# Optimization experiments

Hardware: AMD Instinct MI355X
Metric: run time of the kernel (lower is better)

## Reference

```python
import jax, jax.numpy as jnp
import numpy as np

HEADS = 8
DIM_HEAD = 64
H = W = 32  # height = width = int(sqrt(num_patches)) = 32; n = 1024 tokens
N = H * W
TABLE = (2 * H - 1) * (2 * W - 1)  # 3969
NEG_THRESH = 0.9
GATE = -2.0  # non-trainable gate parameter


def _build_rel_index_dis():
    # valid 2D relative-position index in [0, TABLE) and normalized squared distance
    coords = np.stack(np.meshgrid(np.arange(H), np.arange(W), indexing='ij'))  # (2,H,W)
    flat = coords.reshape(2, -1)  # (2, N)
    rel = flat[:, :, None] - flat[:, None, :]  # (2, N, N)
    dis = (rel[0] / H) ** 2 + (rel[1] / W) ** 2
    idx = (rel[0] + H - 1) * (2 * W - 1) + (rel[1] + W - 1)
    return idx.astype(np.int32), dis.astype(np.float32)


def setup_inputs() -> dict:
    key = jax.random.key(0)
    ks = jax.random.split(key, 8)
    b, n, dim = 4, N, 512
    inner = HEADS * DIM_HEAD
    rel_index, dis = _build_rel_index_dis()
    return {
        'x': jax.random.normal(ks[0], (b, n, dim), jnp.float32),
        'prob': jax.random.uniform(ks[1], (b, n), jnp.float32),
        'W_qkv': jax.random.normal(ks[2], (dim, 3 * inner), jnp.float32) * 0.02,
        'table1': jax.random.normal(ks[3], (TABLE, HEADS), jnp.float32) * 0.02,
        'table2': jax.random.normal(ks[4], (TABLE, HEADS), jnp.float32) * 0.02,
        'headsita': jnp.arange(1, HEADS + 1, dtype=jnp.float32) * 0.1,
        'W_thresh': jax.random.normal(ks[5], (DIM_HEAD, 1), jnp.float32) * 0.02,
        'W_out': jax.random.normal(ks[6], (inner, 512), jnp.float32) * 0.02,
        'b_out': jnp.zeros((512,), jnp.float32),
        'rel_index': jnp.asarray(rel_index),
        'dis': jnp.asarray(dis),
    }


def reference(x, prob, W_qkv, table1, table2, headsita, W_thresh, W_out, b_out, rel_index, dis):
    b, n, dim = x.shape
    scale = DIM_HEAD ** -0.5
    qkv = x @ W_qkv  # (b, n, 3*inner)
    q, k, v = jnp.split(qkv, 3, axis=-1)
    split_heads = lambda t: t.reshape(b, n, HEADS, DIM_HEAD).transpose(0, 2, 1, 3)
    q, k, v = split_heads(q), split_heads(k), split_heads(v)  # (b, h, n, d)

    dots0 = jnp.einsum('bhid,bhjd->bhij', q, k) * scale  # (b, h, n, n)

    # dual RPE bias: product of two table gathers with shared index -> (h, n, n)
    bias = (table1[rel_index] * table2[rel_index]).transpose(2, 0, 1)
    factor = 1.0 / (2.0 * headsita ** 2 + 1e-6)  # (h,)
    pos_embed = jnp.exp(-factor[:, None, None] * dis[None, :, :])  # (h, n, n)
    dots = dots0 + bias[None] + 0.01 * pos_embed[None]

    attn = jax.nn.softmax(dots, axis=-1)
    attn_max = jnp.max(attn, axis=-1)  # (b, h, n)
    attn_min = jnp.min(attn, axis=-1)

    # per-query dynamic threshold, gated
    thresh_raw = jax.nn.sigmoid(jnp.einsum('bhnd,do->bhn', q, W_thresh)) * jax.nn.sigmoid(GATE)
    thresh = attn_min + thresh_raw * (attn_max - attn_min)  # (b, h, n)

    record = (attn - thresh[..., None] > 0).astype(attn.dtype)  # (b, h, n, n)
    # zero out query rows where prob >= NEG_THRESH
    record = jnp.where(prob[:, None, :, None] >= NEG_THRESH, 0.0, record)

    deno = jnp.einsum('bhij,bhij->bhi', attn, record)
    attn_pruned = attn * record / (deno[..., None] + 1e-6)

    out = jnp.einsum('bhij,bhjd->bhid', attn_pruned, v)  # (b, h, n, d)
    out = out.transpose(0, 2, 1, 3).reshape(b, n, HEADS * DIM_HEAD)
    out = out @ W_out + b_out
    attn0 = jax.nn.softmax(dots0, axis=-1)
    return out, attn0
```

## Files before the change

kernel.cpp:

```cpp
#include <hip/hip_runtime.h>
#include <cmath>

#define NTOK 1024
#define NH 8
#define DH 64
#define BATCH 4
#define TBL 3969

#define L2E 1.4426950408889634f

typedef __attribute__((ext_vector_type(8))) short short8;
typedef __attribute__((ext_vector_type(4))) float f32x4;

__device__ __forceinline__ unsigned bf16rne(float x) {
  unsigned u = __float_as_uint(x);
  return (u + 0x7fffu + ((u >> 16) & 1u)) >> 16;
}

__device__ __forceinline__ void cvt2(float a, float b, unsigned& h, unsigned& l) {
  asm("v_cvt_pk_bf16_f32 %0, %1, %2" : "=v"(h) : "v"(a), "v"(b));
  float ra = a - __uint_as_float(h << 16);
  float rb = b - __uint_as_float(h & 0xffff0000u);
  asm("v_cvt_pk_bf16_f32 %0, %1, %2" : "=v"(l) : "v"(ra), "v"(rb));
}

__device__ __forceinline__ void split8_pk(const float* v, short8& h8, short8& l8) {
  union { short8 s; unsigned u[4]; } H, L;
#pragma unroll
  for (int j = 0; j < 4; ++j) {
    unsigned hp, lp;
    cvt2(v[2 * j], v[2 * j + 1], hp, lp);
    H.u[j] = hp; L.u[j] = lp;
  }
  h8 = H.s; l8 = L.s;
}

__device__ __forceinline__ f32x4 mfma16(short8 a, short8 b, f32x4 c) {
  return __builtin_amdgcn_mfma_f32_16x16x32_bf16(a, b, c, 0, 0, 0);
}

__device__ __forceinline__ void gload16(const unsigned short* g, unsigned short* l) {
  __builtin_amdgcn_global_load_lds(
      (__attribute__((address_space(1))) unsigned int*)(g),
      (__attribute__((address_space(3))) unsigned int*)(l), 16, 0, 0);
}

__global__ void k_comb(const float* __restrict__ t1, const float* __restrict__ t2,
                       const float* __restrict__ sita, const float* __restrict__ dis,
                       float* __restrict__ comb, float* __restrict__ combe) {
  int idx = blockIdx.x * 256 + threadIdx.x;
  if (idx >= TBL) return;
  int dy = idx / 63 - 31, dx = idx % 63 - 31;
  int yi = dy > 0 ? dy : 0, yj = dy > 0 ? 0 : -dy;
  int xi = dx > 0 ? dx : 0, xj = dx > 0 ? 0 : -dx;
  float dv = dis[(size_t)(yi * 32 + xi) * NTOK + (yj * 32 + xj)];
#pragma unroll
  for (int h = 0; h < NH; ++h) {
    float ita = sita[h];
    float factor = 1.0f / (2.0f * ita * ita + 1e-6f);
    float bi = t1[idx * 8 + h] * t2[idx * 8 + h];
    float v = bi + 0.01f * expf(-factor * dv);
    comb[(size_t)h * TBL + idx] = v * L2E;
    combe[(size_t)h * TBL + idx] = expf(v);
  }
}

__global__ __launch_bounds__(256) void k_prep(
    const float* __restrict__ x, const float* __restrict__ wqkv,
    const float* __restrict__ wout,
    unsigned short* __restrict__ xh, unsigned short* __restrict__ xl,
    unsigned short* __restrict__ wth, unsigned short* __restrict__ wtl,
    unsigned short* __restrict__ wouth, unsigned short* __restrict__ woutl) {
  const int bid = blockIdx.x;
  const int t = threadIdx.x;
  if (bid < 1024) {
    size_t base = ((size_t)bid * 256 + t) * 8;
    float v8[8];
    *(float4*)(v8) = *(const float4*)(x + base);
    *(float4*)(v8 + 4) = *(const float4*)(x + base + 4);
    short8 h8, l8;
    split8_pk(v8, h8, l8);
    *(short8*)(xh + base) = h8;
    *(short8*)(xl + base) = l8;
    return;
  }
  __shared__ float tile[64][65];
  const float* src;
  unsigned short *dh, *dl;
  int n0, k0, N;
  if (bid < 1216) {
    int b2 = bid - 1024;
    n0 = (b2 % 24) * 64; k0 = (b2 / 24) * 64; N = 1536;
    src = wqkv; dh = wth; dl = wtl;
  } else {
    int b2 = bid - 1216;
    n0 = (b2 % 8) * 64; k0 = (b2 / 8) * 64; N = 512;
    src = wout; dh = wouth; dl = woutl;
  }
#pragma unroll
  for (int l = 0; l < 4; ++l) {
    int idx = t + l * 256;
    int r = idx >> 4, c4 = idx & 15;
    float4 v = *(const float4*)(src + (size_t)(k0 + r) * N + n0 + c4 * 4);
    tile[r][c4 * 4 + 0] = v.x; tile[r][c4 * 4 + 1] = v.y;
    tile[r][c4 * 4 + 2] = v.z; tile[r][c4 * 4 + 3] = v.w;
  }
  __syncthreads();
#pragma unroll
  for (int l = 0; l < 2; ++l) {
    int idx = t + l * 256;
    int n = idx >> 3, c8 = idx & 7;
    float v8[8];
#pragma unroll
    for (int j = 0; j < 8; ++j) v8[j] = tile[c8 * 8 + j][n];
    short8 h8, l8;
    split8_pk(v8, h8, l8);
    *(short8*)(dh + (size_t)(n0 + n) * 512 + k0 + c8 * 8) = h8;
    *(short8*)(dl + (size_t)(n0 + n) * 512 + k0 + c8 * 8) = l8;
  }
}

__device__ __forceinline__ void gemm_core(
    const unsigned short* pAh, const unsigned short* pAl,
    const unsigned short* pBh, const unsigned short* pBl,
    int a0, int b0, int w, int lane, f32x4 acc[4][4],
    unsigned short* AhS, unsigned short* AlS,
    unsigned short* BhS, unsigned short* BlS) {
  const int q = lane >> 4, li = lane & 15;
  const int wr = w >> 1, wc = w & 1;
#pragma unroll 1
  for (int k0 = 0; k0 < 512; k0 += 64) {
#pragma unroll
    for (int l = 0; l < 4; ++l) {
      int idx = w * 256 + l * 64 + lane;
      int row = idx >> 3, u = idx & 7;
      int so = k0 + ((u ^ (row & 7)) * 8);
      int db = (w * 256 + l * 64) * 8;
      gload16(pAh + (size_t)(a0 + row) * 512 + so, AhS + db);
      gload16(pAl + (size_t)(a0 + row) * 512 + so, AlS + db);
      gload16(pBh + (size_t)(b0 + row) * 512 + so, BhS + db);
      gload16(pBl + (size_t)(b0 + row) * 512 + so, BlS + db);
    }
    __syncthreads();
#pragma unroll
    for (int c = 0; c < 2; ++c) {
      short8 aH[4], aL[4], bH[4], bL[4];
#pragma unroll
      for (int mt = 0; mt < 4; ++mt) {
        int row = 64 * wr + 16 * mt + li;
        int ro = row * 64 + (((4 * c + q) ^ (row & 7)) * 8);
        aH[mt] = *(const short8*)(AhS + ro);
        aL[mt] = *(const short8*)(AlS + ro);
        int rowb = 64 * wc + 16 * mt + li;
        int rob = rowb * 64 + (((4 * c + q) ^ (rowb & 7)) * 8);
        bH[mt] = *(const short8*)(BhS + rob);
        bL[mt] = *(const short8*)(BlS + rob);
      }
#pragma unroll
      for (int mt = 0; mt < 4; ++mt)
#pragma unroll
        for (int nt = 0; nt < 4; ++nt) {
          acc[mt][nt] = mfma16(aH[mt], bH[nt], acc[mt][nt]);
          acc[mt][nt] = mfma16(aH[mt], bL[nt], acc[mt][nt]);
          acc[mt][nt] = mfma16(aL[mt], bH[nt], acc[mt][nt]);
        }
    }
    __syncthreads();
  }
}

__global__ __launch_bounds__(256, 2) void k_qkv(
    const unsigned short* __restrict__ xh, const unsigned short* __restrict__ xl,
    const unsigned short* __restrict__ wth, const unsigned short* __restrict__ wtl,
    float* __restrict__ qf, unsigned short* __restrict__ kspl,
    unsigned short* __restrict__ vspl) {
  __shared__ unsigned short AhS[8192], AlS[8192], BhS[8192], BlS[8192];
  const int bid = blockIdx.x;
  const int lin = (bid & 7) * 48 + (bid >> 3);
  const int by = lin / 12, bx = lin % 12;
  const int part = bx >> 2;
  const int t = threadIdx.x;
  const int w = t >> 6, lane = t & 63;
  const int q = lane >> 4, li = lane & 15;
  const int wr = w >> 1, wc = w & 1;
  f32x4 acc[4][4] = {};
  if (part < 2)
    gemm_core(wth, wtl, xh, xl, bx * 128, by * 128, w, lane, acc, AhS, AlS, BhS, BlS);
  else
    gemm_core(xh, xl, wth, wtl, by * 128, bx * 128, w, lane, acc, AhS, AlS, BhS, BlS);

  if (part == 0) {
    int hq = bx * 2 + wr;
#pragma unroll
    for (int nt = 0; nt < 4; ++nt) {
      int tok = by * 128 + 64 * wc + 16 * nt + li;
      int b = tok >> 10, i = tok & 1023;
#pragma unroll
      for (int mt = 0; mt < 4; ++mt) {
        int d0 = 16 * mt + 4 * q;
        float4 v;
        v.x = acc[mt][nt][0]; v.y = acc[mt][nt][1];
        v.z = acc[mt][nt][2]; v.w = acc[mt][nt][3];
        *(float4*)(qf + ((size_t)(b * NH + hq) * NTOK + i) * DH + d0) = v;
      }
    }
  } else if (part == 1) {
    int hq = bx * 2 + wr - 8;
#pragma unroll
    for (int nt = 0; nt < 4; ++nt) {
      int tok = by * 128 + 64 * wc + 16 * nt + li;
      int b = tok >> 10, tile = (tok & 1023) >> 6, tl = tok & 63;
      unsigned short* kb = kspl + ((size_t)((b * NH + hq) * 16 + tile) * 2) * 4096;
#pragma unroll
      for (int mt = 0; mt < 4; ++mt) {
        int d0 = 16 * mt + 4 * q;
        int pu = (d0 >> 3) ^ (tl & 7), off = d0 & 7;
        unsigned h0, h1, l0, l1;
        cvt2(acc[mt][nt][0], acc[mt][nt][1], h0, l0);
        cvt2(acc[mt][nt][2], acc[mt][nt][3], h1, l1);
        *(uint2*)(kb + tl * 64 + pu * 8 + off) = make_uint2(h0, h1);
        *(uint2*)(kb + 4096 + tl * 64 + pu * 8 + off) = make_uint2(l0, l1);
      }
    }
  } else {
    int hq = (bx - 8) * 2 + wc;
#pragma unroll
    for (int mt = 0; mt < 4; ++mt) {
      int tok0 = by * 128 + 64 * wr + 16 * mt + 4 * q;
      int b = tok0 >> 10, tile = (tok0 & 1023) >> 6, tl0 = tok0 & 63;
      int lu = tl0 >> 3, off = tl0 & 7;
#pragma unroll
      for (int nt = 0; nt < 4; ++nt) {
        int d = 16 * nt + li;
        unsigned short* vb = vspl + ((size_t)((b * NH + hq) * 16 + tile) * 2) * 4096;
        int pu = lu ^ (d & 7);
        unsigned h0, h1, l0, l1;
        cvt2(acc[mt][nt][0], acc[mt][nt][1], h0, l0);
        cvt2(acc[mt][nt][2], acc[mt][nt][3], h1, l1);
        *(uint2*)(vb + d * 64 + pu * 8 + off) = make_uint2(h0, h1);
        *(uint2*)(vb + 4096 + d * 64 + pu * 8 + off) = make_uint2(l0, l1);
      }
    }
  }
}

__global__ __launch_bounds__(512, 4) void k_attn(
    const float* __restrict__ qf, const unsigned short* __restrict__ kspl,
    const unsigned short* __restrict__ vspl, const float* __restrict__ prob,
    const float* __restrict__ comb, const float* __restrict__ combe,
    const float* __restrict__ wt,
    float* __restrict__ attn0, unsigned short* __restrict__ oh,
    unsigned short* __restrict__ ol) {
  __shared__ unsigned short KhS[4096], KlS[4096];
  __shared__ unsigned short VhS[4096], VlS[4096];
  __shared__ float PfS[64 * 68];
  __shared__ float2 csS[3 * 64];
  __shared__ float thrS[64];

  const int bid = blockIdx.x;
  const int lin = (bid & 7) * 64 + (bid >> 3);
  const int bh = lin >> 4;
  const int rt = lin & 15;
  const int b = bh >> 3, h = bh & 7;
  const int i0 = rt * 64;
  const int t = threadIdx.x;
  const int w = t >> 6;
  const int lane = t & 63;
  const int q = lane >> 4, li = lane & 15;
  const int g = w >> 1;
  const int cw = w & 1;
  const float* qb = qf + (size_t)bh * NTOK * DH;
  const float* ch = comb + (size_t)h * TBL;
  const float* che = combe + (size_t)h * TBL;
  const int rbase = (i0 >> 5) + 30;

  {
    int row = t >> 3, dg = t & 7;
    const float* qr2 = qb + (size_t)(i0 + row) * DH + dg * 8;
    float sum = 0.f;
#pragma unroll
    for (int c = 0; c < 8; ++c) sum += qr2[c] * wt[dg * 8 + c];
    sum += __shfl_xor(sum, 1);
    sum += __shfl_xor(sum, 2);
    sum += __shfl_xor(sum, 4);
    if (dg == 0)
      thrS[row] = (1.0f / (1.0f + exp2f(-sum * L2E))) * 0.11920292202211755f;
  }

  short8 qah[2], qal[2];
  {
    const float* qr2 = qb + (size_t)(i0 + 16 * g + li) * DH;
    const float QS = 0.125f * L2E;
#pragma unroll
    for (int c = 0; c < 2; ++c) {
      float4 a = *(const float4*)(qr2 + 32 * c + 8 * q);
      float4 bb = *(const float4*)(qr2 + 32 * c + 8 * q + 4);
      float tmp[8] = {a.x * QS, a.y * QS, a.z * QS, a.w * QS,
                      bb.x * QS, bb.y * QS, bb.z * QS, bb.w * QS};
      split8_pk(tmp, qah[c], qal[c]);
    }
  }

  float m0l[4], s0l[4], ml[4], sl[4], mnl[4];
#pragma unroll
  for (int r = 0; r < 4; ++r) {
    m0l[r] = -1e30f; ml[r] = -1e30f; mnl[r] = 1e30f;
    s0l[r] = 0.f; sl[r] = 0.f;
  }

#pragma unroll 1
  for (int j0 = 0; j0 < NTOK; j0 += 64) {
    const unsigned short* gk = kspl + ((size_t)(bh * 16 + (j0 >> 6)) * 2) * 4096;
    gload16(gk + w * 512 + lane * 8, KhS + w * 512);
    gload16(gk + 4096 + w * 512 + lane * 8, KlS + w * 512);
    if (t < 192) {
      int rl2 = t >> 6, c2 = t & 63;
      if (c2 < 63) {
        int off = (rbase - (j0 >> 5) + rl2) * 63 + c2;
        csS[rl2 * 64 + c2] = make_float2(ch[off], che[off]);
      }
    }
    __syncthreads();

    f32x4 acc2[2] = {};
#pragma unroll
    for (int c = 0; c < 2; ++c) {
#pragma unroll
      for (int T2 = 0; T2 < 2; ++T2) {
        int T = 2 * cw + T2;
        int ro = (16 * T + li) * 64 + ((4 * c + q) ^ (li & 7)) * 8;
        short8 bh8 = *(const short8*)(KhS + ro);
        short8 bl8 = *(const short8*)(KlS + ro);
        acc2[T2] = mfma16(qah[c], bh8, acc2[T2]);
        acc2[T2] = mfma16(qah[c], bl8, acc2[T2]);
        acc2[T2] = mfma16(qal[c], bh8, acc2[T2]);
      }
    }

    float2 ce[2][4];
    float t0[4], tt[4], tmn[4];
#pragma unroll
    for (int r = 0; r < 4; ++r) { t0[r] = -1e30f; tt[r] = -1e30f; tmn[r] = 1e30f; }
#pragma unroll
    for (int T2 = 0; T2 < 2; ++T2) {
      int jj = 16 * (2 * cw + T2) + li;
#pragma unroll
      for (int r = 0; r < 4; ++r) {
        int il = 16 * g + 4 * q + r;
        int rl2 = (il >> 5) - (jj >> 5) + 1;
        int cc2 = (il & 31) - (jj & 31) + 31;
        ce[T2][r] = csS[rl2 * 64 + cc2];
        float d0 = acc2[T2][r];
        float dt = d0 + ce[T2][r].x;
        t0[r] = fmaxf(t0[r], d0);
        tt[r] = fmaxf(tt[r], dt);
        tmn[r] = fminf(tmn[r], dt);
      }
    }
#pragma unroll
    for (int r = 0; r < 4; ++r) {
      float nm0 = fmaxf(m0l[r], t0[r]);
      float nm = fmaxf(ml[r], tt[r]);
      float sc0 = exp2f(m0l[r] - nm0), sc = exp2f(ml[r] - nm), k0 = exp2f(nm0 - nm);
      float s0a = 0.f, sEa = 0.f;
#pragma unroll
      for (int T2 = 0; T2 < 2; ++T2) {
        float e0 = exp2f(acc2[T2][r] - nm0);
        s0a += e0;
        sEa += e0 * ce[T2][r].y;
      }
      s0l[r] = s0l[r] * sc0 + s0a;
      sl[r] = sl[r] * sc + sEa * k0;
      m0l[r] = nm0; ml[r] = nm; mnl[r] = fminf(mnl[r], tmn[r]);
    }
    __syncthreads();
  }

  float M0[4], S0[4], M[4], S[4], MN[4];
#pragma unroll
  for (int r = 0; r < 4; ++r) {
    float m0v = m0l[r], s0 = s0l[r], m = ml[r], s = sl[r], mn = mnl[r];
#pragma unroll
    for (int off = 1; off < 16; off <<= 1) {
      float om = __shfl_xor(m0v, off), os = __shfl_xor(s0, off);
      float n0 = fmaxf(m0v, om);
      s0 = s0 * exp2f(m0v - n0) + os * exp2f(om - n0);
      m0v = n0;
      float om2 = __shfl_xor(m, off), os2 = __shfl_xor(s, off);
      float n2 = fmaxf(m, om2);
      s = s * exp2f(m - n2) + os2 * exp2f(om2 - n2);
      m = n2;
      mn = fminf(mn, __shfl_xor(mn, off));
    }
    M0[r] = m0v; S0[r] = s0; M[r] = m; S[r] = s; MN[r] = mn;
  }
  if (li == 0) {
#pragma unroll
    for (int r = 0; r < 4; ++r) {
      int row = 16 * g + 4 * q + r;
      float* p = PfS + (cw * 64 + row) * 5;
      p[0] = M0[r]; p[1] = S0[r]; p[2] = M[r]; p[3] = S[r]; p[4] = MN[r];
    }
  }
  __syncthreads();

  float m0f[4], is0f[4], thf[4], crf[4];
#pragma unroll
  for (int r = 0; r < 4; ++r) {
    int rloc = 16 * g + 4 * q + r;
    const float* pa = PfS + rloc * 5;
    const float* pb = PfS + (64 + rloc) * 5;
    float m0v = fmaxf(pa[0], pb[0]);
    float s0 = pa[1] * exp2f(pa[0] - m0v) + pb[1] * exp2f(pb[0] - m0v);
    float m = fmaxf(pa[2], pb[2]);
    float s = pa[3] * exp2f(pa[2] - m) + pb[3] * exp2f(pb[2] - m);
    float mn = fminf(pa[4], pb[4]);
    float isf = 1.f / s;
    float amin = exp2f(mn - m) * isf;
    float th = amin + thrS[rloc] * (isf - amin);
    if (prob[b * NTOK + i0 + rloc] >= 0.9f) th = 1e30f;
    m0f[r] = m0v; is0f[r] = 1.f / s0; thf[r] = th; crf[r] = exp2f(m0v - m) * isf;
  }
  __syncthreads();

  f32x4 oacc[4] = {};
  float denl[4] = {0.f, 0.f, 0.f, 0.f};
#pragma unroll 1
  for (int j0 = 0; j0 < NTOK; j0 += 64) {
    const unsigned short* gk = kspl + ((size_t)(bh * 16 + (j0 >> 6)) * 2) * 4096;
    const unsigned short* gv = vspl + ((size_t)(bh * 16 + (j0 >> 6)) * 2) * 4096;
    gload16(gk + w * 512 + lane * 8, KhS + w * 512);
    gload16(gk + 4096 + w * 512 + lane * 8, KlS + w * 512);
    gload16(gv + w * 512 + lane * 8, VhS + w * 512);
    gload16(gv + 4096 + w * 512 + lane * 8, VlS + w * 512);
    if (t < 192) {
      int rl2 = t >> 6, c2 = t & 63;
      if (c2 < 63) {
        int off = (rbase - (j0 >> 5) + rl2) * 63 + c2;
        csS[rl2 * 64 + c2] = make_float2(ch[off], che[off]);
      }
    }
    __syncthreads();

    f32x4 acc2[2] = {};
#pragma unroll
    for (int c = 0; c < 2; ++c) {
#pragma unroll
      for (int T2 = 0; T2 < 2; ++T2) {
        int T = 2 * cw + T2;
        int ro = (16 * T + li) * 64 + ((4 * c + q) ^ (li & 7)) * 8;
        short8 bh8 = *(const short8*)(KhS + ro);
        short8 bl8 = *(const short8*)(KlS + ro);
        acc2[T2] = mfma16(qah[c], bh8, acc2[T2]);
        acc2[T2] = mfma16(qah[c], bl8, acc2[T2]);
        acc2[T2] = mfma16(qal[c], bh8, acc2[T2]);
      }
    }

#pragma unroll
    for (int T2 = 0; T2 < 2; ++T2) {
      int jj = 16 * (2 * cw + T2) + li;
#pragma unroll
      for (int r = 0; r < 4; ++r) {
        int il = 16 * g + 4 * q + r;
        int rl2 = (il >> 5) - (jj >> 5) + 1;
        int cc2 = (il & 31) - (jj & 31) + 31;
        float ey = csS[rl2 * 64 + cc2].y;
        float e0 = exp2f(acc2[T2][r] - m0f[r]);
        __builtin_nontemporal_store(
            e0 * is0f[r],
            attn0 + (size_t)(bh * NTOK + i0 + il) * NTOK + j0 + jj);
        float at = e0 * ey * crf[r];
        float p = (at - thf[r] > 0.f) ? at : 0.f;
        denl[r] += p;
        PfS[il * 68 + jj] = p;
      }
    }
    {
      const float* pp = PfS + (16 * g + li) * 68 + 32 * cw + 8 * q;
      float pv8[8];
      *(float4*)(pv8) = *(const float4*)pp;
      *(float4*)(pv8 + 4) = *(const float4*)(pp + 4);
      short8 pah, pal;
      split8_pk(pv8, pah, pal);
#pragma unroll
      for (int T = 0; T < 4; ++T) {
        int ro = (16 * T + li) * 64 + ((4 * cw + q) ^ (li & 7)) * 8;
        short8 vh8 = *(const short8*)(VhS + ro);
        short8 vl8 = *(const short8*)(VlS + ro);
        oacc[T] = mfma16(pah, vh8, oacc[T]);
        oacc[T] = mfma16(pah, vl8, oacc[T]);
        oacc[T] = mfma16(pal, vh8, oacc[T]);
      }
    }
    __syncthreads();
  }

#pragma unroll
  for (int r = 0; r < 4; ++r) {
#pragma unroll
    for (int off = 1; off < 16; off <<= 1) denl[r] += __shfl_xor(denl[r], off);
  }
  if (cw == 1) {
#pragma unroll
    for (int r = 0; r < 4; ++r) {
      int row = 16 * g + 4 * q + r;
#pragma unroll
      for (int T = 0; T < 4; ++T) PfS[row * 68 + 16 * T + li] = oacc[T][r];
      if (li == 0) PfS[row * 68 + 64] = denl[r];
    }
  }
  __syncthreads();
  if (cw == 0) {
#pragma unroll
    for (int r = 0; r < 4; ++r) {
      int rloc = 16 * g + 4 * q + r;
      float dsum = denl[r] + PfS[rloc * 68 + 64];
      float pf = 1.f / (dsum + 1e-6f);
      int row = i0 + rloc;
      size_t rb2 = ((size_t)b * NTOK + row) * 512 + h * 64;
#pragma unroll
      for (int T = 0; T < 4; ++T) {
        float val = (oacc[T][r] + PfS[rloc * 68 + 16 * T + li]) * pf;
        unsigned hv = bf16rne(val);
        float lo2 = val - __uint_as_float(hv << 16);
        oh[rb2 + 16 * T + li] = (unsigned short)hv;
        ol[rb2 + 16 * T + li] = (unsigned short)bf16rne(lo2);
      }
    }
  }
}

__global__ __launch_bounds__(256, 2) void k_out(
    const unsigned short* __restrict__ wouth, const unsigned short* __restrict__ woutl,
    const unsigned short* __restrict__ oh, const unsigned short* __restrict__ ol,
    const float* __restrict__ bias, float* __restrict__ c) {
  __shared__ unsigned short AhS[8192], AlS[8192], BhS[8192], BlS[8192];
  const int bid = blockIdx.x;
  const int lin = (bid & 7) * 16 + (bid >> 3);
  const int by = lin >> 2, bx = lin & 3;
  const int t = threadIdx.x;
  const int w = t >> 6, lane = t & 63;
  const int q = lane >> 4, li = lane & 15;
  const int wr = w >> 1, wc = w & 1;
  f32x4 acc[4][4] = {};
  gemm_core(wouth, woutl, oh, ol, bx * 128, by * 128, w, lane, acc, AhS, AlS, BhS, BlS);
#pragma unroll
  for (int mt = 0; mt < 4; ++mt) {
    int col0 = bx * 128 + 64 * wr + 16 * mt + 4 * q;
    float4 b4 = *(const float4*)(bias + col0);
#pragma unroll
    for (int nt = 0; nt < 4; ++nt) {
      int tok = by * 128 + 64 * wc + 16 * nt + li;
      float4 v;
      v.x = acc[mt][nt][0] + b4.x; v.y = acc[mt][nt][1] + b4.y;
      v.z = acc[mt][nt][2] + b4.z; v.w = acc[mt][nt][3] + b4.w;
      *(float4*)(c + (size_t)tok * 512 + col0) = v;
    }
  }
}

extern "C" void kernel_launch(void* const* d_in, const int* in_sizes, int n_in,
                              void* d_out, int out_size, void* d_ws, size_t ws_size,
                              hipStream_t stream) {
  const float* x    = (const float*)d_in[0];
  const float* prob = (const float*)d_in[1];
  const float* wqkv = (const float*)d_in[2];
  const float* t1   = (const float*)d_in[3];
  const float* t2   = (const float*)d_in[4];
  const float* sita = (const float*)d_in[5];
  const float* wt   = (const float*)d_in[6];
  const float* wout = (const float*)d_in[7];
  const float* bout = (const float*)d_in[8];
  const float* dis  = (const float*)d_in[10];

  float* out = (float*)d_out;
  float* attn0 = out + (size_t)BATCH * NTOK * 512;

  float* comb = (float*)d_ws;
  float* combe = comb + 32768;
  float* qf = combe + 32768;
  unsigned short* kspl = (unsigned short*)(qf + (size_t)BATCH * NH * NTOK * DH);
  unsigned short* vspl = kspl + (size_t)4194304;
  unsigned short* xh = vspl + (size_t)4194304;
  unsigned short* xl = xh + (size_t)2097152;
  unsigned short* wth = xl + (size_t)2097152;
  unsigned short* wtl = wth + (size_t)786432;
  unsigned short* wouth = wtl + (size_t)786432;
  unsigned short* woutl = wouth + (size_t)262144;
  unsigned short* oh = xh;
  unsigned short* ol = xl;

  hipLaunchKernelGGL(k_comb, dim3(16), dim3(256), 0, stream, t1, t2, sita, dis, comb, combe);
  hipLaunchKernelGGL(k_prep, dim3(1280), dim3(256), 0, stream,
                     x, wqkv, wout, xh, xl, wth, wtl, wouth, woutl);
  hipLaunchKernelGGL(k_qkv, dim3(384), dim3(256), 0, stream,
                     xh, xl, wth, wtl, qf, kspl, vspl);
  hipLaunchKernelGGL(k_attn, dim3(512), dim3(512), 0, stream,
                     qf, kspl, vspl, prob, comb, combe, wt, attn0, oh, ol);
  hipLaunchKernelGGL(k_out, dim3(128), dim3(256), 0, stream,
                     wouth, woutl, oh, ol, bout, out);
}
```

Measured before the change: 280.5 us.

## Fuse comb into prep, shrink GEMM tiles, stage attn0 stores through LDS

Folds the comb table kernel into the prep kernel as extra blocks, which removes one launch. Templates the split-bf16 GEMM core so the QKV and output GEMMs can use 64x128 tiles, doubling grid sizes and raising the occupancy hint to 3 so the device has more blocks in flight. The attention kernel now writes the attn0 softmax tile into LDS and then issues coalesced 32-byte nontemporal row stores, instead of scattered per-element stores. It also hoists the relative-position table address math out of the inner loop. The costs are extra LDS use in k_attn, an added barrier, and less data reuse per GEMM tile.

```diff
diff --git a/kernel.cpp b/kernel.cpp
--- a/kernel.cpp
+++ b/kernel.cpp
@@ -45,34 +45,35 @@
       (__attribute__((address_space(3))) unsigned int*)(l), 16, 0, 0);
 }
 
-__global__ void k_comb(const float* __restrict__ t1, const float* __restrict__ t2,
-                       const float* __restrict__ sita, const float* __restrict__ dis,
-                       float* __restrict__ comb, float* __restrict__ combe) {
-  int idx = blockIdx.x * 256 + threadIdx.x;
-  if (idx >= TBL) return;
-  int dy = idx / 63 - 31, dx = idx % 63 - 31;
-  int yi = dy > 0 ? dy : 0, yj = dy > 0 ? 0 : -dy;
-  int xi = dx > 0 ? dx : 0, xj = dx > 0 ? 0 : -dx;
-  float dv = dis[(size_t)(yi * 32 + xi) * NTOK + (yj * 32 + xj)];
-#pragma unroll
-  for (int h = 0; h < NH; ++h) {
-    float ita = sita[h];
-    float factor = 1.0f / (2.0f * ita * ita + 1e-6f);
-    float bi = t1[idx * 8 + h] * t2[idx * 8 + h];
-    float v = bi + 0.01f * expf(-factor * dv);
-    comb[(size_t)h * TBL + idx] = v * L2E;
-    combe[(size_t)h * TBL + idx] = expf(v);
-  }
-}
-
 __global__ __launch_bounds__(256) void k_prep(
     const float* __restrict__ x, const float* __restrict__ wqkv,
     const float* __restrict__ wout,
     unsigned short* __restrict__ xh, unsigned short* __restrict__ xl,
     unsigned short* __restrict__ wth, unsigned short* __restrict__ wtl,
-    unsigned short* __restrict__ wouth, unsigned short* __restrict__ woutl) {
+    unsigned short* __restrict__ wouth, unsigned short* __restrict__ woutl,
+    const float* __restrict__ t1, const float* __restrict__ t2,
+    const float* __restrict__ sita, const float* __restrict__ dis,
+    float* __restrict__ comb, float* __restrict__ combe) {
   const int bid = blockIdx.x;
   const int t = threadIdx.x;
+  if (bid >= 1280) {
+    int idx = (bid - 1280) * 256 + t;
+    if (idx >= TBL) return;
+    int dy = idx / 63 - 31, dx = idx % 63 - 31;
+    int yi = dy > 0 ? dy : 0, yj = dy > 0 ? 0 : -dy;
+    int xi = dx > 0 ? dx : 0, xj = dx > 0 ? 0 : -dx;
+    float dv = dis[(size_t)(yi * 32 + xi) * NTOK + (yj * 32 + xj)];
+#pragma unroll
+    for (int h = 0; h < NH; ++h) {
+      float ita = sita[h];
+      float factor = 1.0f / (2.0f * ita * ita + 1e-6f);
+      float bi = t1[idx * 8 + h] * t2[idx * 8 + h];
+      float v = bi + 0.01f * expf(-factor * dv);
+      comb[(size_t)h * TBL + idx] = v * L2E;
+      combe[(size_t)h * TBL + idx] = expf(v);
+    }
+    return;
+  }
   if (bid < 1024) {
     size_t base = ((size_t)bid * 256 + t) * 8;
     float v8[8];
@@ -120,46 +121,58 @@
   }
 }
 
+template <int AR, int BR>
 __device__ __forceinline__ void gemm_core(
-    const unsigned short* pAh, const unsigned short* pAl,
-    const unsigned short* pBh, const unsigned short* pBl,
-    int a0, int b0, int w, int lane, f32x4 acc[4][4],
+    const unsigned short* __restrict__ pAh, const unsigned short* __restrict__ pAl,
+    const unsigned short* __restrict__ pBh, const unsigned short* __restrict__ pBl,
+    int a0, int b0, int t, f32x4 acc[AR / 32][BR / 32],
     unsigned short* AhS, unsigned short* AlS,
     unsigned short* BhS, unsigned short* BlS) {
+  constexpr int MT = AR / 32, NT = BR / 32;
+  const int lane = t & 63;
+  const int w = t >> 6;
   const int q = lane >> 4, li = lane & 15;
   const int wr = w >> 1, wc = w & 1;
 #pragma unroll 1
   for (int k0 = 0; k0 < 512; k0 += 64) {
 #pragma unroll
-    for (int l = 0; l < 4; ++l) {
-      int idx = w * 256 + l * 64 + lane;
+    for (int l = 0; l < AR / 32; ++l) {
+      int idx = l * 256 + t;
       int row = idx >> 3, u = idx & 7;
       int so = k0 + ((u ^ (row & 7)) * 8);
-      int db = (w * 256 + l * 64) * 8;
-      gload16(pAh + (size_t)(a0 + row) * 512 + so, AhS + db);
-      gload16(pAl + (size_t)(a0 + row) * 512 + so, AlS + db);
-      gload16(pBh + (size_t)(b0 + row) * 512 + so, BhS + db);
-      gload16(pBl + (size_t)(b0 + row) * 512 + so, BlS + db);
+      gload16(pAh + (size_t)(a0 + row) * 512 + so, AhS + idx * 8);
+      gload16(pAl + (size_t)(a0 + row) * 512 + so, AlS + idx * 8);
+    }
+#pragma unroll
+    for (int l = 0; l < BR / 32; ++l) {
+      int idx = l * 256 + t;
+      int row = idx >> 3, u = idx & 7;
+      int so = k0 + ((u ^ (row & 7)) * 8);
+      gload16(pBh + (size_t)(b0 + row) * 512 + so, BhS + idx * 8);
+      gload16(pBl + (size_t)(b0 + row) * 512 + so, BlS + idx * 8);
     }
     __syncthreads();
 #pragma unroll
     for (int c = 0; c < 2; ++c) {
-      short8 aH[4], aL[4], bH[4], bL[4];
-#pragma unroll
-      for (int mt = 0; mt < 4; ++mt) {
-        int row = 64 * wr + 16 * mt + li;
+      short8 aH[MT], aL[MT], bH[NT], bL[NT];
+#pragma unroll
+      for (int mt = 0; mt < MT; ++mt) {
+        int row = (AR / 2) * wr + 16 * mt + li;
         int ro = row * 64 + (((4 * c + q) ^ (row & 7)) * 8);
         aH[mt] = *(const short8*)(AhS + ro);
         aL[mt] = *(const short8*)(AlS + ro);
-        int rowb = 64 * wc + 16 * mt + li;
-        int rob = rowb * 64 + (((4 * c + q) ^ (rowb & 7)) * 8);
-        bH[mt] = *(const short8*)(BhS + rob);
-        bL[mt] = *(const short8*)(BlS + rob);
-      }
-#pragma unroll
-      for (int mt = 0; mt < 4; ++mt)
-#pragma unroll
-        for (int nt = 0; nt < 4; ++nt) {
+      }
+#pragma unroll
+      for (int nt = 0; nt < NT; ++nt) {
+        int row = (BR / 2) * wc + 16 * nt + li;
+        int ro = row * 64 + (((4 * c + q) ^ (row & 7)) * 8);
+        bH[nt] = *(const short8*)(BhS + ro);
+        bL[nt] = *(const short8*)(BlS + ro);
+      }
+#pragma unroll
+      for (int mt = 0; mt < MT; ++mt)
+#pragma unroll
+        for (int nt = 0; nt < NT; ++nt) {
           acc[mt][nt] = mfma16(aH[mt], bH[nt], acc[mt][nt]);
           acc[mt][nt] = mfma16(aH[mt], bL[nt], acc[mt][nt]);
           acc[mt][nt] = mfma16(aL[mt], bH[nt], acc[mt][nt]);
@@ -169,70 +182,72 @@
   }
 }
 
-__global__ __launch_bounds__(256, 2) void k_qkv(
+__global__ __launch_bounds__(256, 3) void k_qkv(
     const unsigned short* __restrict__ xh, const unsigned short* __restrict__ xl,
     const unsigned short* __restrict__ wth, const unsigned short* __restrict__ wtl,
     float* __restrict__ qf, unsigned short* __restrict__ kspl,
     unsigned short* __restrict__ vspl) {
-  __shared__ unsigned short AhS[8192], AlS[8192], BhS[8192], BlS[8192];
+  __shared__ unsigned short S[24576];
   const int bid = blockIdx.x;
-  const int lin = (bid & 7) * 48 + (bid >> 3);
-  const int by = lin / 12, bx = lin % 12;
-  const int part = bx >> 2;
+  const int lin = (bid & 7) * 96 + (bid >> 3);
+  const int by = lin / 24, bx = lin % 24;
+  const int part = bx >> 3, h = bx & 7;
   const int t = threadIdx.x;
-  const int w = t >> 6, lane = t & 63;
+  const int lane = t & 63;
+  const int w = t >> 6;
   const int q = lane >> 4, li = lane & 15;
   const int wr = w >> 1, wc = w & 1;
-  f32x4 acc[4][4] = {};
-  if (part < 2)
-    gemm_core(wth, wtl, xh, xl, bx * 128, by * 128, w, lane, acc, AhS, AlS, BhS, BlS);
-  else
-    gemm_core(xh, xl, wth, wtl, by * 128, bx * 128, w, lane, acc, AhS, AlS, BhS, BlS);
-
-  if (part == 0) {
-    int hq = bx * 2 + wr;
-#pragma unroll
-    for (int nt = 0; nt < 4; ++nt) {
-      int tok = by * 128 + 64 * wc + 16 * nt + li;
-      int b = tok >> 10, i = tok & 1023;
-#pragma unroll
-      for (int mt = 0; mt < 4; ++mt) {
-        int d0 = 16 * mt + 4 * q;
-        float4 v;
-        v.x = acc[mt][nt][0]; v.y = acc[mt][nt][1];
-        v.z = acc[mt][nt][2]; v.w = acc[mt][nt][3];
-        *(float4*)(qf + ((size_t)(b * NH + hq) * NTOK + i) * DH + d0) = v;
-      }
-    }
-  } else if (part == 1) {
-    int hq = bx * 2 + wr - 8;
-#pragma unroll
-    for (int nt = 0; nt < 4; ++nt) {
-      int tok = by * 128 + 64 * wc + 16 * nt + li;
-      int b = tok >> 10, tile = (tok & 1023) >> 6, tl = tok & 63;
-      unsigned short* kb = kspl + ((size_t)((b * NH + hq) * 16 + tile) * 2) * 4096;
-#pragma unroll
-      for (int mt = 0; mt < 4; ++mt) {
-        int d0 = 16 * mt + 4 * q;
-        int pu = (d0 >> 3) ^ (tl & 7), off = d0 & 7;
-        unsigned h0, h1, l0, l1;
-        cvt2(acc[mt][nt][0], acc[mt][nt][1], h0, l0);
-        cvt2(acc[mt][nt][2], acc[mt][nt][3], h1, l1);
-        *(uint2*)(kb + tl * 64 + pu * 8 + off) = make_uint2(h0, h1);
-        *(uint2*)(kb + 4096 + tl * 64 + pu * 8 + off) = make_uint2(l0, l1);
+
+  if (part < 2) {
+    f32x4 acc[2][4] = {};
+    int a0 = part * 512 + h * 64;
+    gemm_core<64, 128>(wth, wtl, xh, xl, a0, by * 128, t, acc,
+                       S, S + 4096, S + 8192, S + 16384);
+    if (part == 0) {
+#pragma unroll
+      for (int nt = 0; nt < 4; ++nt) {
+        int tok = by * 128 + 64 * wc + 16 * nt + li;
+        int b = tok >> 10, i = tok & 1023;
+#pragma unroll
+        for (int mt = 0; mt < 2; ++mt) {
+          int d0 = 32 * wr + 16 * mt + 4 * q;
+          float4 v;
+          v.x = acc[mt][nt][0]; v.y = acc[mt][nt][1];
+          v.z = acc[mt][nt][2]; v.w = acc[mt][nt][3];
+          *(float4*)(qf + ((size_t)(b * NH + h) * NTOK + i) * DH + d0) = v;
+        }
+      }
+    } else {
+#pragma unroll
+      for (int nt = 0; nt < 4; ++nt) {
+        int tok = by * 128 + 64 * wc + 16 * nt + li;
+        int b = tok >> 10, tile = (tok & 1023) >> 6, tl = tok & 63;
+        unsigned short* kb = kspl + ((size_t)((b * NH + h) * 16 + tile) * 2) * 4096;
+#pragma unroll
+        for (int mt = 0; mt < 2; ++mt) {
+          int d0 = 32 * wr + 16 * mt + 4 * q;
+          int pu = (d0 >> 3) ^ (tl & 7), off = d0 & 7;
+          unsigned h0, h1, l0, l1;
+          cvt2(acc[mt][nt][0], acc[mt][nt][1], h0, l0);
+          cvt2(acc[mt][nt][2], acc[mt][nt][3], h1, l1);
+          *(uint2*)(kb + tl * 64 + pu * 8 + off) = make_uint2(h0, h1);
+          *(uint2*)(kb + 4096 + tl * 64 + pu * 8 + off) = make_uint2(l0, l1);
+        }
       }
     }
   } else {
-    int hq = (bx - 8) * 2 + wc;
+    f32x4 acc[4][2] = {};
+    gemm_core<128, 64>(xh, xl, wth, wtl, by * 128, 1024 + h * 64, t, acc,
+                       S, S + 8192, S + 16384, S + 20480);
 #pragma unroll
     for (int mt = 0; mt < 4; ++mt) {
       int tok0 = by * 128 + 64 * wr + 16 * mt + 4 * q;
       int b = tok0 >> 10, tile = (tok0 & 1023) >> 6, tl0 = tok0 & 63;
       int lu = tl0 >> 3, off = tl0 & 7;
-#pragma unroll
-      for (int nt = 0; nt < 4; ++nt) {
-        int d = 16 * nt + li;
-        unsigned short* vb = vspl + ((size_t)((b * NH + hq) * 16 + tile) * 2) * 4096;
+      unsigned short* vb = vspl + ((size_t)((b * NH + h) * 16 + tile) * 2) * 4096;
+#pragma unroll
+      for (int nt = 0; nt < 2; ++nt) {
+        int d = 32 * wc + 16 * nt + li;
         int pu = lu ^ (d & 7);
         unsigned h0, h1, l0, l1;
         cvt2(acc[mt][nt][0], acc[mt][nt][1], h0, l0);
@@ -254,6 +269,7 @@
   __shared__ unsigned short KhS[4096], KlS[4096];
   __shared__ unsigned short VhS[4096], VlS[4096];
   __shared__ float PfS[64 * 68];
+  __shared__ float A0S[64 * 68];
   __shared__ float2 csS[3 * 64];
   __shared__ float thrS[64];
 
@@ -344,12 +360,12 @@
 #pragma unroll
     for (int T2 = 0; T2 < 2; ++T2) {
       int jj = 16 * (2 * cw + T2) + li;
+      int rl2 = (g >> 1) - (jj >> 5) + 1;
+      int cb = 16 * (g & 1) + 4 * q - (jj & 31) + 31;
+      const float2* cp = csS + rl2 * 64 + cb;
 #pragma unroll
       for (int r = 0; r < 4; ++r) {
-        int il = 16 * g + 4 * q + r;
-        int rl2 = (il >> 5) - (jj >> 5) + 1;
-        int cc2 = (il & 31) - (jj & 31) + 31;
-        ce[T2][r] = csS[rl2 * 64 + cc2];
+        ce[T2][r] = cp[r];
         float d0 = acc2[T2][r];
         float dt = d0 + ce[T2][r].x;
         t0[r] = fmaxf(t0[r], d0);
@@ -376,7 +392,7 @@
     __syncthreads();
   }
 
-  float M0[4], S0[4], M[4], S[4], MN[4];
+  float M0[4], S0v[4], M[4], Sv[4], MN[4];
 #pragma unroll
   for (int r = 0; r < 4; ++r) {
     float m0v = m0l[r], s0 = s0l[r], m = ml[r], s = sl[r], mn = mnl[r];
@@ -392,14 +408,14 @@
       m = n2;
       mn = fminf(mn, __shfl_xor(mn, off));
     }
-    M0[r] = m0v; S0[r] = s0; M[r] = m; S[r] = s; MN[r] = mn;
+    M0[r] = m0v; S0v[r] = s0; M[r] = m; Sv[r] = s; MN[r] = mn;
   }
   if (li == 0) {
 #pragma unroll
     for (int r = 0; r < 4; ++r) {
       int row = 16 * g + 4 * q + r;
       float* p = PfS + (cw * 64 + row) * 5;
-      p[0] = M0[r]; p[1] = S0[r]; p[2] = M[r]; p[3] = S[r]; p[4] = MN[r];
+      p[0] = M0[r]; p[1] = S0v[r]; p[2] = M[r]; p[3] = Sv[r]; p[4] = MN[r];
     }
   }
   __syncthreads();
@@ -460,16 +476,16 @@
 #pragma unroll
     for (int T2 = 0; T2 < 2; ++T2) {
       int jj = 16 * (2 * cw + T2) + li;
+      int rl2 = (g >> 1) - (jj >> 5) + 1;
+      int cb = 16 * (g & 1) + 4 * q - (jj & 31) + 31;
+      const float2* cp = csS + rl2 * 64 + cb;
+      int il0 = 16 * g + 4 * q;
 #pragma unroll
       for (int r = 0; r < 4; ++r) {
-        int il = 16 * g + 4 * q + r;
-        int rl2 = (il >> 5) - (jj >> 5) + 1;
-        int cc2 = (il & 31) - (jj & 31) + 31;
-        float ey = csS[rl2 * 64 + cc2].y;
+        float ey = cp[r].y;
         float e0 = exp2f(acc2[T2][r] - m0f[r]);
-        __builtin_nontemporal_store(
-            e0 * is0f[r],
-            attn0 + (size_t)(bh * NTOK + i0 + il) * NTOK + j0 + jj);
+        int il = il0 + r;
+        A0S[il * 68 + jj] = e0 * is0f[r];
         float at = e0 * ey * crf[r];
         float p = (at - thf[r] > 0.f) ? at : 0.f;
         denl[r] += p;
@@ -494,6 +510,15 @@
       }
     }
     __syncthreads();
+    {
+      int row = t >> 3, c8 = (t & 7) * 8;
+      const float* src = A0S + row * 68 + c8;
+      f32x4 v0 = *(const f32x4*)src;
+      f32x4 v1 = *(const f32x4*)(src + 4);
+      float* dst = attn0 + (size_t)(bh * NTOK + i0 + row) * NTOK + j0 + c8;
+      __builtin_nontemporal_store(v0, (f32x4*)dst);
+      __builtin_nontemporal_store(v1, (f32x4*)(dst + 4));
+    }
   }
 
 #pragma unroll
@@ -501,6 +526,7 @@
 #pragma unroll
     for (int off = 1; off < 16; off <<= 1) denl[r] += __shfl_xor(denl[r], off);
   }
+  __syncthreads();
   if (cw == 1) {
 #pragma unroll
     for (int r = 0; r < 4; ++r) {
@@ -531,23 +557,25 @@
   }
 }
 
-__global__ __launch_bounds__(256, 2) void k_out(
+__global__ __launch_bounds__(256, 3) void k_out(
     const unsigned short* __restrict__ wouth, const unsigned short* __restrict__ woutl,
     const unsigned short* __restrict__ oh, const unsigned short* __restrict__ ol,
     const float* __restrict__ bias, float* __restrict__ c) {
-  __shared__ unsigned short AhS[8192], AlS[8192], BhS[8192], BlS[8192];
+  __shared__ unsigned short S[24576];
   const int bid = blockIdx.x;
-  const int lin = (bid & 7) * 16 + (bid >> 3);
-  const int by = lin >> 2, bx = lin & 3;
+  const int lin = (bid & 7) * 32 + (bid >> 3);
+  const int by = lin >> 3, bx = lin & 7;
   const int t = threadIdx.x;
-  const int w = t >> 6, lane = t & 63;
+  const int lane = t & 63;
+  const int w = t >> 6;
   const int q = lane >> 4, li = lane & 15;
   const int wr = w >> 1, wc = w & 1;
-  f32x4 acc[4][4] = {};
-  gemm_core(wouth, woutl, oh, ol, bx * 128, by * 128, w, lane, acc, AhS, AlS, BhS, BlS);
-#pragma unroll
-  for (int mt = 0; mt < 4; ++mt) {
-    int col0 = bx * 128 + 64 * wr + 16 * mt + 4 * q;
+  f32x4 acc[2][4] = {};
+  gemm_core<64, 128>(wouth, woutl, oh, ol, bx * 64, by * 128, t, acc,
+                     S, S + 4096, S + 8192, S + 16384);
+#pragma unroll
+  for (int mt = 0; mt < 2; ++mt) {
+    int col0 = bx * 64 + 32 * wr + 16 * mt + 4 * q;
     float4 b4 = *(const float4*)(bias + col0);
 #pragma unroll
     for (int nt = 0; nt < 4; ++nt) {
@@ -591,13 +619,13 @@
   unsigned short* oh = xh;
   unsigned short* ol = xl;
 
-  hipLaunchKernelGGL(k_comb, dim3(16), dim3(256), 0, stream, t1, t2, sita, dis, comb, combe);
-  hipLaunchKernelGGL(k_prep, dim3(1280), dim3(256), 0, stream,
-                     x, wqkv, wout, xh, xl, wth, wtl, wouth, woutl);
-  hipLaunchKernelGGL(k_qkv, dim3(384), dim3(256), 0, stream,
+  hipLaunchKernelGGL(k_prep, dim3(1296), dim3(256), 0, stream,
+                     x, wqkv, wout, xh, xl, wth, wtl, wouth, woutl,
+                     t1, t2, sita, dis, comb, combe);
+  hipLaunchKernelGGL(k_qkv, dim3(768), dim3(256), 0, stream,
                      xh, xl, wth, wtl, qf, kspl, vspl);
   hipLaunchKernelGGL(k_attn, dim3(512), dim3(512), 0, stream,
                      qf, kspl, vspl, prob, comb, combe, wt, attn0, oh, ol);
-  hipLaunchKernelGGL(k_out, dim3(128), dim3(256), 0, stream,
+  hipLaunchKernelGGL(k_out, dim3(256), dim3(256), 0, stream,
                      wouth, woutl, oh, ol, bout, out);
 }
```

Result: no change. 286.0 us (+2.0%).
